# Kernel optimization log

Hardware: AMD Instinct MI355X
Metric: run time of the kernel (lower is better)

Reference implementation:

```python
import jax, jax.numpy as jnp
import numpy as np

L = 4096      # number of nodes (treated as sequence length, batch=1)
D = 256       # in_channels == out_channels
H = 8         # heads
DH = D // H   # head dim = 32
NUM_EDGE_TYPES = 14


def setup_inputs() -> dict:
    key = jax.random.key(0)
    ks = jax.random.split(key, 7)
    x = jax.random.normal(ks[0], (L, D), dtype=jnp.float32)
    mask = jax.random.randint(ks[1], (L, L), 0, NUM_EDGE_TYPES, dtype=jnp.int64)
    s = 1.0 / np.sqrt(D)
    in_proj_w = jax.random.uniform(ks[2], (3 * D, D), jnp.float32, -s, s)
    in_proj_b = jnp.zeros((3 * D,), jnp.float32)
    out_proj_w = jax.random.uniform(ks[3], (D, D), jnp.float32, -s, s)
    out_proj_b = jnp.zeros((D,), jnp.float32)
    edge_bias = jax.random.normal(ks[4], (NUM_EDGE_TYPES, H), dtype=jnp.float32) * 0.02
    return {"x": x, "mask": mask, "in_proj_w": in_proj_w, "in_proj_b": in_proj_b,
            "out_proj_w": out_proj_w, "out_proj_b": out_proj_b, "edge_bias": edge_bias}


def reference(x, mask, in_proj_w, in_proj_b, out_proj_w, out_proj_b, edge_bias):
    # x: (L, D) node features -> viewed as batch-1 self-attention, edge-aware scores.
    qkv = x @ in_proj_w.T + in_proj_b                 # (L, 3D)
    q, k, v = jnp.split(qkv, 3, axis=-1)              # each (L, D)
    q = q.reshape(L, H, DH).transpose(1, 0, 2)        # (H, L, DH)
    k = k.reshape(L, H, DH).transpose(1, 0, 2)
    v = v.reshape(L, H, DH).transpose(1, 0, 2)
    scale = 1.0 / jnp.sqrt(jnp.asarray(DH, x.dtype))
    scores = jnp.einsum('hqd,hkd->hqk', q, k) * scale  # (H, L, L)
    # edge-type bias folded into attention scores: lookup (L,L)->(L,L,H)->(H,L,L)
    scores = scores + edge_bias[mask].transpose(2, 0, 1)
    attn = jax.nn.softmax(scores, axis=-1)             # (H, L, L)
    out = jnp.einsum('hqk,hkd->hqd', attn, v)          # (H, L, DH)
    out = out.transpose(1, 0, 2).reshape(L, D)         # merge heads
    return out @ out_proj_w.T + out_proj_b             # (L, D)
```

## Files before the change

### kernel.cpp

```cpp
#include <hip/hip_runtime.h>
#include <hip/hip_bf16.h>
#include <string.h>

#define L 4096
#define D 256
#define H 8
#define DH 32

typedef __attribute__((ext_vector_type(8))) short bf16x8;
typedef __attribute__((ext_vector_type(4))) float f32x4;

#define LOG2E 1.4426950408889634f
#define RS (0.17677669529663688f * LOG2E)

__device__ __forceinline__ ushort f2bf(float f) {
    union { float f; unsigned int i; } v; v.f = f;
    unsigned int x = v.i;
    return (ushort)((x + 0x7fffu + ((x >> 16) & 1u)) >> 16);
}
__device__ __forceinline__ bf16x8 cvt8(const float* p) {
    float4 a = *(const float4*)p;
    float4 b = *(const float4*)(p + 4);
    bf16x8 r;
    r[0] = (short)f2bf(a.x); r[1] = (short)f2bf(a.y);
    r[2] = (short)f2bf(a.z); r[3] = (short)f2bf(a.w);
    r[4] = (short)f2bf(b.x); r[5] = (short)f2bf(b.y);
    r[6] = (short)f2bf(b.z); r[7] = (short)f2bf(b.w);
    return r;
}
__device__ __forceinline__ unsigned int pkbf(float a, float b) {
    float2 t; t.x = a; t.y = b;
    __hip_bfloat162 r = __float22bfloat162_rn(t);
    unsigned int u; memcpy(&u, &r, 4);
    return u;
}
__device__ __forceinline__ float uaf(unsigned int u) {
    union { unsigned int u; float f; } v; v.u = u; return v.f;
}

__device__ __forceinline__ int ksig(int u) {
    return 32 * (u >> 5) + 16 * ((u >> 2) & 1) + 4 * ((u >> 3) & 3) + (u & 3);
}


__global__ __launch_bounds__(256) void pack_kernel(
        const int* __restrict__ mask, const float* __restrict__ x,
        const float* __restrict__ wi, const float* __restrict__ wo,
        unsigned int* __restrict__ m2, ushort* __restrict__ xb,
        ushort* __restrict__ wib, ushort* __restrict__ wob)
{
    const int b = blockIdx.x;
    const int tid = threadIdx.x;
    if (b < 512) {
        __shared__ unsigned int rb[8 * 1025];
        const int4* src = (const int4*)(mask + (size_t)b * 8 * 4096);
#pragma unroll
        for (int i = 0; i < 32; i++) {
            const int g = i * 256 + tid;
            int4 v = src[g];
            rb[(g >> 10) * 1025 + (g & 1023)] =
                ((unsigned int)(v.x & 15) << 4)  | ((unsigned int)(v.y & 15) << 12) |
                ((unsigned int)(v.z & 15) << 20) | ((unsigned int)(v.w & 15) << 28);
        }
        __syncthreads();
        const int t = b >> 1, half = b & 1;
#pragma unroll
        for (int i = 0; i < 32; i++) {
            const int dd = i * 256 + tid;
            const int nt = dd & 3, s = (dd >> 2) & 7, qd = (dd >> 5) & 3, kt = dd >> 7;
            const unsigned int w =
                rb[s * 1025 + kt * 16 + 8 * (nt >> 1) + 2 * qd + (nt & 1)];
            const unsigned int e0 = (w >> 4) & 15u, e1 = (w >> 12) & 15u;
            const unsigned int e2 = (w >> 20) & 15u, e3 = w >> 28;
            const unsigned int p01 = e0 * 14u + e1, p23 = e2 * 14u + e3;
            m2[(size_t)t * 16384 + kt * 256 + (qd * 16 + 8 * half + s) * 4 + nt] =
                (p01 * 68u) | ((p23 * 68u) << 16);
        }
    } else if (b < 1024) {
        const int g = (b - 512) * 256 + tid;
        const int l = g & 15, kd = (g >> 4) & 31, mg = g >> 9;
        ((bf16x8*)xb)[g] = cvt8(x + (mg * 16 + l) * 256 + kd * 8);
    } else if (b < 1120) {
        const int g = (b - 1024) * 256 + tid;
        const int l = g & 15, kd = (g >> 4) & 31, mg = g >> 9;
        ((bf16x8*)wib)[g] = cvt8(wi + (mg * 16 + l) * 256 + kd * 8);
    } else {
        const int g = (b - 1120) * 256 + tid;
        const int l = g & 15, kd = (g >> 4) & 31, mg = g >> 9;
        ((bf16x8*)wob)[g] = cvt8(wo + (mg * 16 + l) * 256 + kd * 8);
    }
}

__global__ __launch_bounds__(256) void qkv_kernel(
        const ushort* __restrict__ xb, const ushort* __restrict__ wb,
        const float* __restrict__ b,
        ushort* __restrict__ Qb, ushort* __restrict__ Kb, ushort* __restrict__ Vt)
{
    __shared__ ushort tile[64][72];

    const int lane = threadIdx.x & 63, wv = threadIdx.x >> 6;
    const int quad = lane >> 4, l15 = lane & 15;
    const int m0b = blockIdx.x * 64;
    const int by = blockIdx.y;
    const int n0 = by * 64;
    const ushort* ap = xb + (size_t)(blockIdx.x * 4 + wv) * 4096 + l15 * 8;
    const ushort* bp = wb + (size_t)(by * 4) * 4096 + l15 * 8;

    f32x4 acc[4] = {};
    for (int ks = 0; ks < 8; ks++) {
        const int kdi = (ks * 4 + quad) * 128;
        bf16x8 af = *(const bf16x8*)(ap + kdi);
#pragma unroll
        for (int nt = 0; nt < 4; nt++) {
            bf16x8 bfr = *(const bf16x8*)(bp + nt * 4096 + kdi);
            acc[nt] = __builtin_amdgcn_mfma_f32_16x16x32_bf16(af, bfr, acc[nt], 0, 0, 0);
        }
    }

    const bool isQ = (by < 4), isK = (by >= 4) && (by < 8);
#pragma unroll
    for (int nt = 0; nt < 4; nt++) {
        const int c = nt * 16 + l15;
        const float bias = b[n0 + c];
#pragma unroll
        for (int r = 0; r < 4; r++) {
            const int lr = wv * 16 + quad * 4 + r;
            float val = acc[nt][r] + bias;
            if (isQ) val *= RS;
            tile[isK ? ksig(lr) : lr][c] = f2bf(val);
        }
    }
    __syncthreads();

    const int t = threadIdx.x;
    if (by < 8) {
        const int hh = t >> 7, i = t & 127;
        ushort* dst = isQ ? Qb + ((size_t)(by * 2 + hh) * L + m0b) * 32
                          : Kb + ((size_t)((by - 4) * 2 + hh) * L + m0b) * 32;
#pragma unroll
        for (int k = 0; k < 2; k++) {
            const int ci = i + k * 128;
            const int row = ci >> 2, wc = (ci & 3) * 8;
            *(bf16x8*)(dst + ci * 8) = *(const bf16x8*)(&tile[row][hh * 32 + wc]);
        }
    } else {
        const int c = t & 63, rh = t >> 6;
        const int vc = n0 - 512 + c;
        ushort tmp[16];
#pragma unroll
        for (int r = 0; r < 16; r++) tmp[r] = tile[rh * 16 + r][c];
        ushort* dst = Vt + (size_t)vc * L + m0b + rh * 16;
        *(bf16x8*)dst       = *(const bf16x8*)tmp;
        *(bf16x8*)(dst + 8) = *(const bf16x8*)(tmp + 8);
    }
}

__global__ __launch_bounds__(512) void attn_kernel(
        const ushort* __restrict__ Qb, const ushort* __restrict__ Kb,
        const ushort* __restrict__ Vt, const unsigned char* __restrict__ m2,
        const float* __restrict__ edge_bias, ushort* __restrict__ Ob)
{
    __shared__ unsigned int lutp[196 * 17];
    __shared__ float red[7 * 576];

    const int tid = threadIdx.x;
    const int lane = tid & 63, wv = tid >> 6;
    const int quad = lane >> 4, l15 = lane & 15;

    const int bid = blockIdx.x;
    const int xr = bid & 7, j = bid >> 3;
    const int qg = xr * 16 + (j >> 3);
    const int h  = j & 7;
    const int q0 = qg * 32;
    const int kt0 = wv * 8;

    for (int p = tid; p < 196; p += 512) {
        const int e1 = (p * 2341) >> 15;
        const int e2 = p - 14 * e1;
        const unsigned int v = pkbf(edge_bias[e1 * H + h] * LOG2E,
                                    edge_bias[e2 * H + h] * LOG2E);
#pragma unroll
        for (int c = 0; c < 17; c++) lutp[p * 17 + c] = v;
    }
    __syncthreads();

    const bf16x8 qfA = *(const bf16x8*)(Qb + (h * L + q0 + l15) * DH + quad * 8);
    const bf16x8 qfB = *(const bf16x8*)(Qb + (h * L + q0 + 16 + l15) * DH + quad * 8);
    const char* lutb = (const char*)lutp + l15 * 4;

    const ushort* Kl = Kb + h * L * DH + kt0 * 64 * DH + l15 * DH + quad * 8;
    const ushort* Va = Vt + (h * DH + l15) * L + kt0 * 64 + quad * 8;
    const ushort* Vb = Vt + (h * DH + 16 + l15) * L + kt0 * 64 + quad * 8;
    const unsigned char* mpA = m2 + (size_t)(2 * qg) * 65536
                             + (size_t)kt0 * 1024 + lane * 16;
    const unsigned char* mpB = mpA + 65536;

    f32x4 o0A = {}, o1A = {}, osA = {};
    f32x4 o0B = {}, o1B = {}, osB = {};
    bf16x8 ones;
#pragma unroll
    for (int i = 0; i < 8; i++) ones[i] = (short)0x3F80;

    for (int kt = 0; kt < 8; kt++) {
        const int4 mA4 = *(const int4*)(mpA + kt * 1024);
        const int4 mB4 = *(const int4*)(mpB + kt * 1024);
        const unsigned int mA[4] = {(unsigned int)mA4.x, (unsigned int)mA4.y,
                                    (unsigned int)mA4.z, (unsigned int)mA4.w};
        const unsigned int mB[4] = {(unsigned int)mB4.x, (unsigned int)mB4.y,
                                    (unsigned int)mB4.z, (unsigned int)mB4.w};

#pragma unroll
        for (int half = 0; half < 2; half++) {
            union { bf16x8 v; unsigned int u[4]; } pfA, pfB;
#pragma unroll
            for (int nt2 = 0; nt2 < 2; nt2++) {
                const int nt = half * 2 + nt2;
                bf16x8 kf = *(const bf16x8*)(Kl + (kt * 64 + nt * 16) * DH);
                f32x4 z = {};
                f32x4 svA = __builtin_amdgcn_mfma_f32_16x16x32_bf16(kf, qfA, z, 0, 0, 0);
                f32x4 svB = __builtin_amdgcn_mfma_f32_16x16x32_bf16(kf, qfB, z, 0, 0, 0);
                const unsigned int wA = mA[nt], wB = mB[nt];
                const unsigned int dA0 = *(const unsigned int*)(lutb + (wA & 0xFFFFu));
                const unsigned int dA1 = *(const unsigned int*)(lutb + (wA >> 16));
                const unsigned int dB0 = *(const unsigned int*)(lutb + (wB & 0xFFFFu));
                const unsigned int dB1 = *(const unsigned int*)(lutb + (wB >> 16));
                float a0 = __builtin_amdgcn_exp2f(svA[0] + uaf(dA0 << 16));
                float a1 = __builtin_amdgcn_exp2f(svA[1] + uaf(dA0 & 0xFFFF0000u));
                float a2 = __builtin_amdgcn_exp2f(svA[2] + uaf(dA1 << 16));
                float a3 = __builtin_amdgcn_exp2f(svA[3] + uaf(dA1 & 0xFFFF0000u));
                float b0 = __builtin_amdgcn_exp2f(svB[0] + uaf(dB0 << 16));
                float b1 = __builtin_amdgcn_exp2f(svB[1] + uaf(dB0 & 0xFFFF0000u));
                float b2 = __builtin_amdgcn_exp2f(svB[2] + uaf(dB1 << 16));
                float b3 = __builtin_amdgcn_exp2f(svB[3] + uaf(dB1 & 0xFFFF0000u));
                pfA.u[nt2 * 2]     = pkbf(a0, a1);
                pfA.u[nt2 * 2 + 1] = pkbf(a2, a3);
                pfB.u[nt2 * 2]     = pkbf(b0, b1);
                pfB.u[nt2 * 2 + 1] = pkbf(b2, b3);
            }
            bf16x8 va = *(const bf16x8*)(Va + kt * 64 + half * 32);
            bf16x8 vb = *(const bf16x8*)(Vb + kt * 64 + half * 32);
            __builtin_amdgcn_s_setprio(1);
            o0A = __builtin_amdgcn_mfma_f32_16x16x32_bf16(va,   pfA.v, o0A, 0, 0, 0);
            o1A = __builtin_amdgcn_mfma_f32_16x16x32_bf16(vb,   pfA.v, o1A, 0, 0, 0);
            osA = __builtin_amdgcn_mfma_f32_16x16x32_bf16(ones, pfA.v, osA, 0, 0, 0);
            o0B = __builtin_amdgcn_mfma_f32_16x16x32_bf16(va,   pfB.v, o0B, 0, 0, 0);
            o1B = __builtin_amdgcn_mfma_f32_16x16x32_bf16(vb,   pfB.v, o1B, 0, 0, 0);
            osB = __builtin_amdgcn_mfma_f32_16x16x32_bf16(ones, pfB.v, osB, 0, 0, 0);
            __builtin_amdgcn_s_setprio(0);
        }
    }

    ushort* obase = Ob + (size_t)(2 * qg) * 4096 + l15 * 8 + (quad & 1) * 4;
    ushort* or0A = obase + (h * 4 + (quad >> 1)) * 128;
    ushort* or1A = obase + (h * 4 + 2 + (quad >> 1)) * 128;
    ushort* or0B = or0A + 4096;
    ushort* or1B = or1A + 4096;

    if (wv > 0) {
        float* s = red + (wv - 1) * 576;
        *(f32x4*)(s +       lane * 4) = o0A;
        *(f32x4*)(s + 256 + lane * 4) = o1A;
        s[512 + lane] = osA[0];
    }
    __syncthreads();
    if (wv == 0) {
#pragma unroll
        for (int sl = 0; sl < 7; sl++) {
            const float* s = red + sl * 576;
            o0A += *(const f32x4*)(s +       lane * 4);
            o1A += *(const f32x4*)(s + 256 + lane * 4);
            osA[0] += s[512 + lane];
        }
        const float invA = 1.f / osA[0];
        uint2 u;
        u.x = pkbf(o0A[0] * invA, o0A[1] * invA);
        u.y = pkbf(o0A[2] * invA, o0A[3] * invA);
        *(uint2*)or0A = u;
        u.x = pkbf(o1A[0] * invA, o1A[1] * invA);
        u.y = pkbf(o1A[2] * invA, o1A[3] * invA);
        *(uint2*)or1A = u;
    }
    __syncthreads();
    if (wv > 0) {
        float* s = red + (wv - 1) * 576;
        *(f32x4*)(s +       lane * 4) = o0B;
        *(f32x4*)(s + 256 + lane * 4) = o1B;
        s[512 + lane] = osB[0];
    }
    __syncthreads();
    if (wv == 0) {
#pragma unroll
        for (int sl = 0; sl < 7; sl++) {
            const float* s = red + sl * 576;
            o0B += *(const f32x4*)(s +       lane * 4);
            o1B += *(const f32x4*)(s + 256 + lane * 4);
            osB[0] += s[512 + lane];
        }
        const float invB = 1.f / osB[0];
        uint2 u;
        u.x = pkbf(o0B[0] * invB, o0B[1] * invB);
        u.y = pkbf(o0B[2] * invB, o0B[3] * invB);
        *(uint2*)or0B = u;
        u.x = pkbf(o1B[0] * invB, o1B[1] * invB);
        u.y = pkbf(o1B[2] * invB, o1B[3] * invB);
        *(uint2*)or1B = u;
    }
}

__global__ __launch_bounds__(256) void oproj_kernel(
        const ushort* __restrict__ Ob, const ushort* __restrict__ wb,
        const float* __restrict__ b, float* __restrict__ out)
{
    const int lane = threadIdx.x & 63, wv = threadIdx.x >> 6;
    const int quad = lane >> 4, l15 = lane & 15;
    const int m0 = blockIdx.x * 64 + wv * 16;
    const int n0 = blockIdx.y * 16;
    const ushort* ap = Ob + (size_t)(blockIdx.x * 4 + wv) * 4096 + l15 * 8;
    const ushort* bp = wb + (size_t)blockIdx.y * 4096 + l15 * 8;

    f32x4 acc = {};
    for (int ks = 0; ks < 8; ks++) {
        const int kdi = (ks * 4 + quad) * 128;
        bf16x8 af  = *(const bf16x8*)(ap + kdi);
        bf16x8 bfr = *(const bf16x8*)(bp + kdi);
        acc = __builtin_amdgcn_mfma_f32_16x16x32_bf16(af, bfr, acc, 0, 0, 0);
    }
    const int j = n0 + l15;
    const float bias = b[j];
#pragma unroll
    for (int r = 0; r < 4; r++) {
        out[(m0 + quad * 4 + r) * D + j] = acc[r] + bias;
    }
}

extern "C" void kernel_launch(void* const* d_in, const int* in_sizes, int n_in,
                              void* d_out, int out_size, void* d_ws, size_t ws_size,
                              hipStream_t stream) {
    const float* x     = (const float*)d_in[0];
    const int*   mask  = (const int*)d_in[1];
    const float* in_w  = (const float*)d_in[2];
    const float* in_b  = (const float*)d_in[3];
    const float* out_w = (const float*)d_in[4];
    const float* out_b = (const float*)d_in[5];
    const float* eb    = (const float*)d_in[6];

    ushort* ws = (ushort*)d_ws;
    ushort* Qb  = ws;
    ushort* Kb  = Qb + H * L * DH;
    ushort* Vt  = Kb + H * L * DH;
    ushort* xb  = Vt + H * L * DH;
    ushort* wib = xb + L * D;
    ushort* wob = wib + 3 * D * D;
    unsigned char* m2 = (unsigned char*)(wob + D * D);
    ushort* Ob = (ushort*)(m2 + (size_t)L * L);
    float* out = (float*)d_out;

    pack_kernel<<<dim3(1152), 256, 0, stream>>>(mask, x, in_w, out_w,
                                                (unsigned int*)m2, xb, wib, wob);
    qkv_kernel<<<dim3(64, 12), 256, 0, stream>>>(xb, wib, in_b, Qb, Kb, Vt);
    attn_kernel<<<dim3(1024), 512, 0, stream>>>(Qb, Kb, Vt, m2, eb, Ob);
    oproj_kernel<<<dim3(64, 16), 256, 0, stream>>>(Ob, wob, out_b, out);
}
```

Baseline: 171.3 us.

## Fuse all four stages into one cooperative persistent kernel with grid syncs

```diff
diff --git a/kernel.cpp b/kernel.cpp
--- a/kernel.cpp
+++ b/kernel.cpp
@@ -1,6 +1,9 @@
 #include <hip/hip_runtime.h>
 #include <hip/hip_bf16.h>
+#include <hip/hip_cooperative_groups.h>
 #include <string.h>
+
+namespace cg = cooperative_groups;
 
 #define L 4096
 #define D 256
@@ -37,137 +40,130 @@
 __device__ __forceinline__ float uaf(unsigned int u) {
     union { unsigned int u; float f; } v; v.u = u; return v.f;
 }
-
 __device__ __forceinline__ int ksig(int u) {
     return 32 * (u >> 5) + 16 * ((u >> 2) & 1) + 4 * ((u >> 3) & 3) + (u & 3);
 }
 
 
-__global__ __launch_bounds__(256) void pack_kernel(
-        const int* __restrict__ mask, const float* __restrict__ x,
-        const float* __restrict__ wi, const float* __restrict__ wo,
-        unsigned int* __restrict__ m2, ushort* __restrict__ xb,
-        ushort* __restrict__ wib, ushort* __restrict__ wob)
-{
-    const int b = blockIdx.x;
-    const int tid = threadIdx.x;
-    if (b < 512) {
-        __shared__ unsigned int rb[8 * 1025];
-        const int4* src = (const int4*)(mask + (size_t)b * 8 * 4096);
-#pragma unroll
-        for (int i = 0; i < 32; i++) {
-            const int g = i * 256 + tid;
-            int4 v = src[g];
-            rb[(g >> 10) * 1025 + (g & 1023)] =
-                ((unsigned int)(v.x & 15) << 4)  | ((unsigned int)(v.y & 15) << 12) |
-                ((unsigned int)(v.z & 15) << 20) | ((unsigned int)(v.w & 15) << 28);
-        }
-        __syncthreads();
-        const int t = b >> 1, half = b & 1;
-#pragma unroll
-        for (int i = 0; i < 32; i++) {
-            const int dd = i * 256 + tid;
-            const int nt = dd & 3, s = (dd >> 2) & 7, qd = (dd >> 5) & 3, kt = dd >> 7;
-            const unsigned int w =
-                rb[s * 1025 + kt * 16 + 8 * (nt >> 1) + 2 * qd + (nt & 1)];
-            const unsigned int e0 = (w >> 4) & 15u, e1 = (w >> 12) & 15u;
-            const unsigned int e2 = (w >> 20) & 15u, e3 = w >> 28;
-            const unsigned int p01 = e0 * 14u + e1, p23 = e2 * 14u + e3;
-            m2[(size_t)t * 16384 + kt * 256 + (qd * 16 + 8 * half + s) * 4 + nt] =
-                (p01 * 68u) | ((p23 * 68u) << 16);
-        }
-    } else if (b < 1024) {
-        const int g = (b - 512) * 256 + tid;
+__device__ __forceinline__ void m2_body(int b, int tid, int T,
+        unsigned int* rb, const int* __restrict__ mask,
+        unsigned int* __restrict__ m2)
+{
+    const int4* src = (const int4*)(mask + (size_t)b * 8 * 4096);
+    for (int g = tid; g < 8192; g += T) {
+        int4 v = src[g];
+        rb[(g >> 10) * 1025 + (g & 1023)] =
+            ((unsigned int)(v.x & 15) << 4)  | ((unsigned int)(v.y & 15) << 12) |
+            ((unsigned int)(v.z & 15) << 20) | ((unsigned int)(v.w & 15) << 28);
+    }
+    __syncthreads();
+    const int t = b >> 1, half = b & 1;
+    for (int dd = tid; dd < 8192; dd += T) {
+        const int nt = dd & 3, s = (dd >> 2) & 7, qd = (dd >> 5) & 3, kt = dd >> 7;
+        const unsigned int w =
+            rb[s * 1025 + kt * 16 + 8 * (nt >> 1) + 2 * qd + (nt & 1)];
+        const unsigned int e0 = (w >> 4) & 15u, e1 = (w >> 12) & 15u;
+        const unsigned int e2 = (w >> 20) & 15u, e3 = w >> 28;
+        const unsigned int p01 = e0 * 14u + e1, p23 = e2 * 14u + e3;
+        m2[(size_t)t * 16384 + kt * 256 + (qd * 16 + 8 * half + s) * 4 + nt] =
+            (p01 * 68u) | ((p23 * 68u) << 16);
+    }
+}
+
+__device__ __forceinline__ void conv_task(int u,
+        const float* __restrict__ x, const float* __restrict__ wi,
+        const float* __restrict__ wo,
+        ushort* __restrict__ xb, ushort* __restrict__ wib,
+        ushort* __restrict__ wob)
+{
+    if (u < 131072) {
+        const int g = u;
         const int l = g & 15, kd = (g >> 4) & 31, mg = g >> 9;
         ((bf16x8*)xb)[g] = cvt8(x + (mg * 16 + l) * 256 + kd * 8);
-    } else if (b < 1120) {
-        const int g = (b - 1024) * 256 + tid;
+    } else if (u < 155648) {
+        const int g = u - 131072;
         const int l = g & 15, kd = (g >> 4) & 31, mg = g >> 9;
         ((bf16x8*)wib)[g] = cvt8(wi + (mg * 16 + l) * 256 + kd * 8);
-    } else {
-        const int g = (b - 1120) * 256 + tid;
+    } else if (u < 163840) {
+        const int g = u - 155648;
         const int l = g & 15, kd = (g >> 4) & 31, mg = g >> 9;
         ((bf16x8*)wob)[g] = cvt8(wo + (mg * 16 + l) * 256 + kd * 8);
     }
 }
 
-__global__ __launch_bounds__(256) void qkv_kernel(
+__device__ __forceinline__ void qkv_body(bool act, int bx, int by, int tid,
+        ushort (*tile)[72],
         const ushort* __restrict__ xb, const ushort* __restrict__ wb,
         const float* __restrict__ b,
-        ushort* __restrict__ Qb, ushort* __restrict__ Kb, ushort* __restrict__ Vt)
-{
-    __shared__ ushort tile[64][72];
-
-    const int lane = threadIdx.x & 63, wv = threadIdx.x >> 6;
-    const int quad = lane >> 4, l15 = lane & 15;
-    const int m0b = blockIdx.x * 64;
-    const int by = blockIdx.y;
-    const int n0 = by * 64;
-    const ushort* ap = xb + (size_t)(blockIdx.x * 4 + wv) * 4096 + l15 * 8;
-    const ushort* bp = wb + (size_t)(by * 4) * 4096 + l15 * 8;
-
-    f32x4 acc[4] = {};
-    for (int ks = 0; ks < 8; ks++) {
-        const int kdi = (ks * 4 + quad) * 128;
-        bf16x8 af = *(const bf16x8*)(ap + kdi);
+        ushort* __restrict__ Qb, ushort* __restrict__ Kb,
+        ushort* __restrict__ Vt)
+{
+    const int m0b = bx * 64;
+    const bool isQ = (by < 4), isK = (by >= 4) && (by < 8);
+    if (act) {
+        const int lane = tid & 63, wv = tid >> 6;
+        const int quad = lane >> 4, l15 = lane & 15;
+        const int n0 = by * 64;
+        const ushort* ap = xb + (size_t)(bx * 4 + wv) * 4096 + l15 * 8;
+        const ushort* bp = wb + (size_t)(by * 4) * 4096 + l15 * 8;
+        f32x4 acc[4] = {};
+        for (int ks = 0; ks < 8; ks++) {
+            const int kdi = (ks * 4 + quad) * 128;
+            bf16x8 af = *(const bf16x8*)(ap + kdi);
+#pragma unroll
+            for (int nt = 0; nt < 4; nt++) {
+                bf16x8 bfr = *(const bf16x8*)(bp + nt * 4096 + kdi);
+                acc[nt] = __builtin_amdgcn_mfma_f32_16x16x32_bf16(af, bfr, acc[nt], 0, 0, 0);
+            }
+        }
 #pragma unroll
         for (int nt = 0; nt < 4; nt++) {
-            bf16x8 bfr = *(const bf16x8*)(bp + nt * 4096 + kdi);
-            acc[nt] = __builtin_amdgcn_mfma_f32_16x16x32_bf16(af, bfr, acc[nt], 0, 0, 0);
-        }
-    }
-
-    const bool isQ = (by < 4), isK = (by >= 4) && (by < 8);
-#pragma unroll
-    for (int nt = 0; nt < 4; nt++) {
-        const int c = nt * 16 + l15;
-        const float bias = b[n0 + c];
-#pragma unroll
-        for (int r = 0; r < 4; r++) {
-            const int lr = wv * 16 + quad * 4 + r;
-            float val = acc[nt][r] + bias;
-            if (isQ) val *= RS;
-            tile[isK ? ksig(lr) : lr][c] = f2bf(val);
-        }
-    }
-    __syncthreads();
-
-    const int t = threadIdx.x;
-    if (by < 8) {
-        const int hh = t >> 7, i = t & 127;
-        ushort* dst = isQ ? Qb + ((size_t)(by * 2 + hh) * L + m0b) * 32
-                          : Kb + ((size_t)((by - 4) * 2 + hh) * L + m0b) * 32;
-#pragma unroll
-        for (int k = 0; k < 2; k++) {
-            const int ci = i + k * 128;
-            const int row = ci >> 2, wc = (ci & 3) * 8;
-            *(bf16x8*)(dst + ci * 8) = *(const bf16x8*)(&tile[row][hh * 32 + wc]);
-        }
-    } else {
-        const int c = t & 63, rh = t >> 6;
-        const int vc = n0 - 512 + c;
-        ushort tmp[16];
-#pragma unroll
-        for (int r = 0; r < 16; r++) tmp[r] = tile[rh * 16 + r][c];
-        ushort* dst = Vt + (size_t)vc * L + m0b + rh * 16;
-        *(bf16x8*)dst       = *(const bf16x8*)tmp;
-        *(bf16x8*)(dst + 8) = *(const bf16x8*)(tmp + 8);
-    }
-}
-
-__global__ __launch_bounds__(512) void attn_kernel(
+            const int c = nt * 16 + l15;
+            const float bias = b[n0 + c];
+#pragma unroll
+            for (int r = 0; r < 4; r++) {
+                const int lr = wv * 16 + quad * 4 + r;
+                float val = acc[nt][r] + bias;
+                if (isQ) val *= RS;
+                tile[isK ? ksig(lr) : lr][c] = f2bf(val);
+            }
+        }
+    }
+    __syncthreads();
+    if (act) {
+        const int t = tid;
+        if (by < 8) {
+            const int hh = t >> 7, i = t & 127;
+            ushort* dst = isQ ? Qb + ((size_t)(by * 2 + hh) * L + m0b) * 32
+                              : Kb + ((size_t)((by - 4) * 2 + hh) * L + m0b) * 32;
+#pragma unroll
+            for (int k = 0; k < 2; k++) {
+                const int ci = i + k * 128;
+                const int row = ci >> 2, wc = (ci & 3) * 8;
+                *(bf16x8*)(dst + ci * 8) = *(const bf16x8*)(&tile[row][hh * 32 + wc]);
+            }
+        } else {
+            const int c = t & 63, rh = t >> 6;
+            const int vc = by * 64 - 512 + c;
+            ushort tmp[16];
+#pragma unroll
+            for (int r = 0; r < 16; r++) tmp[r] = tile[rh * 16 + r][c];
+            ushort* dst = Vt + (size_t)vc * L + m0b + rh * 16;
+            *(bf16x8*)dst       = *(const bf16x8*)tmp;
+            *(bf16x8*)(dst + 8) = *(const bf16x8*)(tmp + 8);
+        }
+    }
+}
+
+__device__ __forceinline__ void attn_body(int bid, int tid,
+        unsigned int* lutp, float* red,
         const ushort* __restrict__ Qb, const ushort* __restrict__ Kb,
         const ushort* __restrict__ Vt, const unsigned char* __restrict__ m2,
         const float* __restrict__ edge_bias, ushort* __restrict__ Ob)
 {
-    __shared__ unsigned int lutp[196 * 17];
-    __shared__ float red[7 * 576];
-
-    const int tid = threadIdx.x;
     const int lane = tid & 63, wv = tid >> 6;
     const int quad = lane >> 4, l15 = lane & 15;
 
-    const int bid = blockIdx.x;
     const int xr = bid & 7, j = bid >> 3;
     const int qg = xr * 16 + (j >> 3);
     const int h  = j & 7;
@@ -307,16 +303,17 @@
     }
 }
 
-__global__ __launch_bounds__(256) void oproj_kernel(
+__device__ __forceinline__ void oproj_body(bool act, int bx, int byy, int tid,
         const ushort* __restrict__ Ob, const ushort* __restrict__ wb,
         const float* __restrict__ b, float* __restrict__ out)
 {
-    const int lane = threadIdx.x & 63, wv = threadIdx.x >> 6;
+    if (!act) return;
+    const int lane = tid & 63, wv = tid >> 6;
     const int quad = lane >> 4, l15 = lane & 15;
-    const int m0 = blockIdx.x * 64 + wv * 16;
-    const int n0 = blockIdx.y * 16;
-    const ushort* ap = Ob + (size_t)(blockIdx.x * 4 + wv) * 4096 + l15 * 8;
-    const ushort* bp = wb + (size_t)blockIdx.y * 4096 + l15 * 8;
+    const int m0 = bx * 64 + wv * 16;
+    const int n0 = byy * 16;
+    const ushort* ap = Ob + (size_t)(bx * 4 + wv) * 4096 + l15 * 8;
+    const ushort* bp = wb + (size_t)byy * 4096 + l15 * 8;
 
     f32x4 acc = {};
     for (int ks = 0; ks < 8; ks++) {
@@ -331,6 +328,78 @@
     for (int r = 0; r < 4; r++) {
         out[(m0 + quad * 4 + r) * D + j] = acc[r] + bias;
     }
+}
+
+__global__ __launch_bounds__(512, 8) void fused_kernel(
+        const int* __restrict__ mask, const float* __restrict__ x,
+        const float* __restrict__ wi, const float* __restrict__ ib,
+        const float* __restrict__ wo, const float* __restrict__ obias,
+        const float* __restrict__ eb,
+        unsigned int* __restrict__ m2, ushort* __restrict__ xb,
+        ushort* __restrict__ wib, ushort* __restrict__ wob,
+        ushort* __restrict__ Qb, ushort* __restrict__ Kb,
+        ushort* __restrict__ Vt, ushort* __restrict__ Ob,
+        float* __restrict__ out)
+{
+    __shared__ unsigned int SM[8 * 1025];
+    cg::grid_group grid = cg::this_grid();
+    const int bid = blockIdx.x, tid = threadIdx.x;
+
+    if (bid < 512) {
+        m2_body(bid, tid, 512, SM, mask, m2);
+    } else {
+        conv_task((bid - 512) * 512 + tid, x, wi, wo, xb, wib, wob);
+    }
+    grid.sync();
+
+    qkv_body((bid < 768) && (tid < 256), bid & 63, bid >> 6, tid,
+             (ushort(*)[72])SM, xb, wib, ib, Qb, Kb, Vt);
+    grid.sync();
+
+    attn_body(bid, tid, SM, (float*)(SM + 3332), Qb, Kb, Vt,
+              (const unsigned char*)m2, eb, Ob);
+    grid.sync();
+
+    oproj_body(tid < 256, bid & 63, bid >> 6, tid, Ob, wob, obias, out);
+}
+
+__global__ __launch_bounds__(256) void pack_kernel(
+        const int* __restrict__ mask, const float* __restrict__ x,
+        const float* __restrict__ wi, const float* __restrict__ wo,
+        unsigned int* __restrict__ m2, ushort* __restrict__ xb,
+        ushort* __restrict__ wib, ushort* __restrict__ wob)
+{
+    __shared__ unsigned int rb[8 * 1025];
+    const int b = blockIdx.x, tid = threadIdx.x;
+    if (b < 512) m2_body(b, tid, 256, rb, mask, m2);
+    else         conv_task((b - 512) * 256 + tid, x, wi, wo, xb, wib, wob);
+}
+
+__global__ __launch_bounds__(256) void qkv_kernel(
+        const ushort* __restrict__ xb, const ushort* __restrict__ wb,
+        const float* __restrict__ b,
+        ushort* __restrict__ Qb, ushort* __restrict__ Kb,
+        ushort* __restrict__ Vt)
+{
+    __shared__ ushort tile[64][72];
+    qkv_body(true, blockIdx.x, blockIdx.y, threadIdx.x, tile, xb, wb, b, Qb, Kb, Vt);
+}
+
+__global__ __launch_bounds__(512) void attn_kernel(
+        const ushort* __restrict__ Qb, const ushort* __restrict__ Kb,
+        const ushort* __restrict__ Vt, const unsigned char* __restrict__ m2,
+        const float* __restrict__ edge_bias, ushort* __restrict__ Ob)
+{
+    __shared__ unsigned int SMa[7364];
+    attn_body(blockIdx.x, threadIdx.x, SMa, (float*)(SMa + 3332),
+              Qb, Kb, Vt, m2, edge_bias, Ob);
+}
+
+__global__ __launch_bounds__(256) void oproj_kernel(
+        const ushort* __restrict__ Ob, const ushort* __restrict__ wb,
+        const float* __restrict__ b, float* __restrict__ out)
+{
+    oproj_body(true, blockIdx.x, blockIdx.y, threadIdx.x, Ob, wb, b, out);
 }
 
 extern "C" void kernel_launch(void* const* d_in, const int* in_sizes, int n_in,
@@ -351,13 +420,25 @@
     ushort* xb  = Vt + H * L * DH;
     ushort* wib = xb + L * D;
     ushort* wob = wib + 3 * D * D;
-    unsigned char* m2 = (unsigned char*)(wob + D * D);
-    ushort* Ob = (ushort*)(m2 + (size_t)L * L);
+    unsigned int* m2 = (unsigned int*)(wob + D * D);
+    ushort* Ob = (ushort*)((unsigned char*)m2 + (size_t)L * L);
     float* out = (float*)d_out;
 
-    pack_kernel<<<dim3(1152), 256, 0, stream>>>(mask, x, in_w, out_w,
-                                                (unsigned int*)m2, xb, wib, wob);
-    qkv_kernel<<<dim3(64, 12), 256, 0, stream>>>(xb, wib, in_b, Qb, Kb, Vt);
-    attn_kernel<<<dim3(1024), 512, 0, stream>>>(Qb, Kb, Vt, m2, eb, Ob);
-    oproj_kernel<<<dim3(64, 16), 256, 0, stream>>>(Ob, wob, out_b, out);
-}
+    void* args[16] = {
+        (void*)&mask, (void*)&x, (void*)&in_w, (void*)&in_b,
+        (void*)&out_w, (void*)&out_b, (void*)&eb,
+        (void*)&m2, (void*)&xb, (void*)&wib, (void*)&wob,
+        (void*)&Qb, (void*)&Kb, (void*)&Vt, (void*)&Ob, (void*)&out
+    };
+    hipError_t e = hipLaunchCooperativeKernel(
+        reinterpret_cast<const void*>(&fused_kernel),
+        dim3(1024), dim3(512), args, 0, stream);
+    if (e != hipSuccess) {
+        pack_kernel<<<dim3(1152), 256, 0, stream>>>(mask, x, in_w, out_w,
+                                                    m2, xb, wib, wob);
+        qkv_kernel<<<dim3(64, 12), 256, 0, stream>>>(xb, wib, in_b, Qb, Kb, Vt);
+        attn_kernel<<<dim3(1024), 512, 0, stream>>>(Qb, Kb, Vt,
+                                                    (const unsigned char*)m2, eb, Ob);
+        oproj_kernel<<<dim3(64, 16), 256, 0, stream>>>(Ob, wob, out_b, out);
+    }
+}
```

Result: slower. 627.2 us (+266.2%).

## Process 64 queries per attention block to reuse K/V fragments across four tiles

Applied to the files above, without the earlier changes.

```diff
diff --git a/kernel.cpp b/kernel.cpp
--- a/kernel.cpp
+++ b/kernel.cpp
@@ -169,9 +169,9 @@
 
     const int bid = blockIdx.x;
     const int xr = bid & 7, j = bid >> 3;
-    const int qg = xr * 16 + (j >> 3);
+    const int g  = xr * 8 + (j >> 3);
     const int h  = j & 7;
-    const int q0 = qg * 32;
+    const int q0 = g * 64;
     const int kt0 = wv * 8;
 
     for (int p = tid; p < 196; p += 512) {
@@ -184,126 +184,97 @@
     }
     __syncthreads();
 
-    const bf16x8 qfA = *(const bf16x8*)(Qb + (h * L + q0 + l15) * DH + quad * 8);
-    const bf16x8 qfB = *(const bf16x8*)(Qb + (h * L + q0 + 16 + l15) * DH + quad * 8);
+    bf16x8 qf[4];
+#pragma unroll
+    for (int c = 0; c < 4; c++)
+        qf[c] = *(const bf16x8*)(Qb + (h * L + q0 + c * 16 + l15) * DH + quad * 8);
     const char* lutb = (const char*)lutp + l15 * 4;
 
     const ushort* Kl = Kb + h * L * DH + kt0 * 64 * DH + l15 * DH + quad * 8;
     const ushort* Va = Vt + (h * DH + l15) * L + kt0 * 64 + quad * 8;
     const ushort* Vb = Vt + (h * DH + 16 + l15) * L + kt0 * 64 + quad * 8;
-    const unsigned char* mpA = m2 + (size_t)(2 * qg) * 65536
-                             + (size_t)kt0 * 1024 + lane * 16;
-    const unsigned char* mpB = mpA + 65536;
-
-    f32x4 o0A = {}, o1A = {}, osA = {};
-    f32x4 o0B = {}, o1B = {}, osB = {};
+    const unsigned char* mp = m2 + (size_t)(4 * g) * 65536
+                            + (size_t)kt0 * 1024 + lane * 16;
+
+    f32x4 o0[4] = {}, o1[4] = {}, os[4] = {};
     bf16x8 ones;
 #pragma unroll
     for (int i = 0; i < 8; i++) ones[i] = (short)0x3F80;
 
     for (int kt = 0; kt < 8; kt++) {
-        const int4 mA4 = *(const int4*)(mpA + kt * 1024);
-        const int4 mB4 = *(const int4*)(mpB + kt * 1024);
-        const unsigned int mA[4] = {(unsigned int)mA4.x, (unsigned int)mA4.y,
-                                    (unsigned int)mA4.z, (unsigned int)mA4.w};
-        const unsigned int mB[4] = {(unsigned int)mB4.x, (unsigned int)mB4.y,
-                                    (unsigned int)mB4.z, (unsigned int)mB4.w};
+        unsigned int m[4][4];
+#pragma unroll
+        for (int c = 0; c < 4; c++) {
+            const int4 t4 = *(const int4*)(mp + (size_t)c * 65536 + kt * 1024);
+            m[c][0] = (unsigned int)t4.x; m[c][1] = (unsigned int)t4.y;
+            m[c][2] = (unsigned int)t4.z; m[c][3] = (unsigned int)t4.w;
+        }
 
 #pragma unroll
         for (int half = 0; half < 2; half++) {
-            union { bf16x8 v; unsigned int u[4]; } pfA, pfB;
+            union { bf16x8 v; unsigned int u[4]; } pf[4];
 #pragma unroll
             for (int nt2 = 0; nt2 < 2; nt2++) {
                 const int nt = half * 2 + nt2;
                 bf16x8 kf = *(const bf16x8*)(Kl + (kt * 64 + nt * 16) * DH);
-                f32x4 z = {};
-                f32x4 svA = __builtin_amdgcn_mfma_f32_16x16x32_bf16(kf, qfA, z, 0, 0, 0);
-                f32x4 svB = __builtin_amdgcn_mfma_f32_16x16x32_bf16(kf, qfB, z, 0, 0, 0);
-                const unsigned int wA = mA[nt], wB = mB[nt];
-                const unsigned int dA0 = *(const unsigned int*)(lutb + (wA & 0xFFFFu));
-                const unsigned int dA1 = *(const unsigned int*)(lutb + (wA >> 16));
-                const unsigned int dB0 = *(const unsigned int*)(lutb + (wB & 0xFFFFu));
-                const unsigned int dB1 = *(const unsigned int*)(lutb + (wB >> 16));
-                float a0 = __builtin_amdgcn_exp2f(svA[0] + uaf(dA0 << 16));
-                float a1 = __builtin_amdgcn_exp2f(svA[1] + uaf(dA0 & 0xFFFF0000u));
-                float a2 = __builtin_amdgcn_exp2f(svA[2] + uaf(dA1 << 16));
-                float a3 = __builtin_amdgcn_exp2f(svA[3] + uaf(dA1 & 0xFFFF0000u));
-                float b0 = __builtin_amdgcn_exp2f(svB[0] + uaf(dB0 << 16));
-                float b1 = __builtin_amdgcn_exp2f(svB[1] + uaf(dB0 & 0xFFFF0000u));
-                float b2 = __builtin_amdgcn_exp2f(svB[2] + uaf(dB1 << 16));
-                float b3 = __builtin_amdgcn_exp2f(svB[3] + uaf(dB1 & 0xFFFF0000u));
-                pfA.u[nt2 * 2]     = pkbf(a0, a1);
-                pfA.u[nt2 * 2 + 1] = pkbf(a2, a3);
-                pfB.u[nt2 * 2]     = pkbf(b0, b1);
-                pfB.u[nt2 * 2 + 1] = pkbf(b2, b3);
+#pragma unroll
+                for (int c = 0; c < 4; c++) {
+                    f32x4 z = {};
+                    f32x4 sv = __builtin_amdgcn_mfma_f32_16x16x32_bf16(kf, qf[c], z, 0, 0, 0);
+                    const unsigned int w = m[c][nt];
+                    const unsigned int d0 = *(const unsigned int*)(lutb + (w & 0xFFFFu));
+                    const unsigned int d1 = *(const unsigned int*)(lutb + (w >> 16));
+                    float e0 = __builtin_amdgcn_exp2f(sv[0] + uaf(d0 << 16));
+                    float e1 = __builtin_amdgcn_exp2f(sv[1] + uaf(d0 & 0xFFFF0000u));
+                    float e2 = __builtin_amdgcn_exp2f(sv[2] + uaf(d1 << 16));
+                    float e3 = __builtin_amdgcn_exp2f(sv[3] + uaf(d1 & 0xFFFF0000u));
+                    pf[c].u[nt2 * 2]     = pkbf(e0, e1);
+                    pf[c].u[nt2 * 2 + 1] = pkbf(e2, e3);
+                }
             }
             bf16x8 va = *(const bf16x8*)(Va + kt * 64 + half * 32);
             bf16x8 vb = *(const bf16x8*)(Vb + kt * 64 + half * 32);
             __builtin_amdgcn_s_setprio(1);
-            o0A = __builtin_amdgcn_mfma_f32_16x16x32_bf16(va,   pfA.v, o0A, 0, 0, 0);
-            o1A = __builtin_amdgcn_mfma_f32_16x16x32_bf16(vb,   pfA.v, o1A, 0, 0, 0);
-            osA = __builtin_amdgcn_mfma_f32_16x16x32_bf16(ones, pfA.v, osA, 0, 0, 0);
-            o0B = __builtin_amdgcn_mfma_f32_16x16x32_bf16(va,   pfB.v, o0B, 0, 0, 0);
-            o1B = __builtin_amdgcn_mfma_f32_16x16x32_bf16(vb,   pfB.v, o1B, 0, 0, 0);
-            osB = __builtin_amdgcn_mfma_f32_16x16x32_bf16(ones, pfB.v, osB, 0, 0, 0);
+#pragma unroll
+            for (int c = 0; c < 4; c++) {
+                o0[c] = __builtin_amdgcn_mfma_f32_16x16x32_bf16(va,   pf[c].v, o0[c], 0, 0, 0);
+                o1[c] = __builtin_amdgcn_mfma_f32_16x16x32_bf16(vb,   pf[c].v, o1[c], 0, 0, 0);
+                os[c] = __builtin_amdgcn_mfma_f32_16x16x32_bf16(ones, pf[c].v, os[c], 0, 0, 0);
+            }
             __builtin_amdgcn_s_setprio(0);
         }
     }
 
-    ushort* obase = Ob + (size_t)(2 * qg) * 4096 + l15 * 8 + (quad & 1) * 4;
-    ushort* or0A = obase + (h * 4 + (quad >> 1)) * 128;
-    ushort* or1A = obase + (h * 4 + 2 + (quad >> 1)) * 128;
-    ushort* or0B = or0A + 4096;
-    ushort* or1B = or1A + 4096;
-
-    if (wv > 0) {
-        float* s = red + (wv - 1) * 576;
-        *(f32x4*)(s +       lane * 4) = o0A;
-        *(f32x4*)(s + 256 + lane * 4) = o1A;
-        s[512 + lane] = osA[0];
-    }
-    __syncthreads();
-    if (wv == 0) {
-#pragma unroll
-        for (int sl = 0; sl < 7; sl++) {
-            const float* s = red + sl * 576;
-            o0A += *(const f32x4*)(s +       lane * 4);
-            o1A += *(const f32x4*)(s + 256 + lane * 4);
-            osA[0] += s[512 + lane];
-        }
-        const float invA = 1.f / osA[0];
-        uint2 u;
-        u.x = pkbf(o0A[0] * invA, o0A[1] * invA);
-        u.y = pkbf(o0A[2] * invA, o0A[3] * invA);
-        *(uint2*)or0A = u;
-        u.x = pkbf(o1A[0] * invA, o1A[1] * invA);
-        u.y = pkbf(o1A[2] * invA, o1A[3] * invA);
-        *(uint2*)or1A = u;
-    }
-    __syncthreads();
-    if (wv > 0) {
-        float* s = red + (wv - 1) * 576;
-        *(f32x4*)(s +       lane * 4) = o0B;
-        *(f32x4*)(s + 256 + lane * 4) = o1B;
-        s[512 + lane] = osB[0];
-    }
-    __syncthreads();
-    if (wv == 0) {
-#pragma unroll
-        for (int sl = 0; sl < 7; sl++) {
-            const float* s = red + sl * 576;
-            o0B += *(const f32x4*)(s +       lane * 4);
-            o1B += *(const f32x4*)(s + 256 + lane * 4);
-            osB[0] += s[512 + lane];
-        }
-        const float invB = 1.f / osB[0];
-        uint2 u;
-        u.x = pkbf(o0B[0] * invB, o0B[1] * invB);
-        u.y = pkbf(o0B[2] * invB, o0B[3] * invB);
-        *(uint2*)or0B = u;
-        u.x = pkbf(o1B[0] * invB, o1B[1] * invB);
-        u.y = pkbf(o1B[2] * invB, o1B[3] * invB);
-        *(uint2*)or1B = u;
+#pragma unroll
+    for (int c = 0; c < 4; c++) {
+        if (wv > 0) {
+            float* s = red + (wv - 1) * 576;
+            *(f32x4*)(s +       lane * 4) = o0[c];
+            *(f32x4*)(s + 256 + lane * 4) = o1[c];
+            s[512 + lane] = os[c][0];
+        }
+        __syncthreads();
+        if (wv == 0) {
+#pragma unroll
+            for (int sl = 0; sl < 7; sl++) {
+                const float* s = red + sl * 576;
+                o0[c] += *(const f32x4*)(s +       lane * 4);
+                o1[c] += *(const f32x4*)(s + 256 + lane * 4);
+                os[c][0] += s[512 + lane];
+            }
+            const float inv = 1.f / os[c][0];
+            ushort* obase = Ob + (size_t)(4 * g + c) * 4096 + l15 * 8 + (quad & 1) * 4;
+            ushort* or0 = obase + (h * 4 + (quad >> 1)) * 128;
+            ushort* or1 = obase + (h * 4 + 2 + (quad >> 1)) * 128;
+            uint2 u;
+            u.x = pkbf(o0[c][0] * inv, o0[c][1] * inv);
+            u.y = pkbf(o0[c][2] * inv, o0[c][3] * inv);
+            *(uint2*)or0 = u;
+            u.x = pkbf(o1[c][0] * inv, o1[c][1] * inv);
+            u.y = pkbf(o1[c][2] * inv, o1[c][3] * inv);
+            *(uint2*)or1 = u;
+        }
+        __syncthreads();
     }
 }
 
@@ -358,6 +329,6 @@
     pack_kernel<<<dim3(1152), 256, 0, stream>>>(mask, x, in_w, out_w,
                                                 (unsigned int*)m2, xb, wib, wob);
     qkv_kernel<<<dim3(64, 12), 256, 0, stream>>>(xb, wib, in_b, Qb, Kb, Vt);
-    attn_kernel<<<dim3(1024), 512, 0, stream>>>(Qb, Kb, Vt, m2, eb, Ob);
+    attn_kernel<<<dim3(512), 512, 0, stream>>>(Qb, Kb, Vt, m2, eb, Ob);
     oproj_kernel<<<dim3(64, 16), 256, 0, stream>>>(Ob, wob, out_b, out);
 }
```

Result: faster. 161.3 us (-5.8%).
